# Kernel optimization log

Measured on AMD Instinct MI355X. Metric: run time of the kernel, lower is better.

Reference implementation:

```python
import jax, jax.numpy as jnp
import numpy as np

V = 49152      # HEALPix nside=64 pixel count
B = 2
FIN = 32
FOUT = 64
K = 8          # Chebyshev kernel_size
DEG = 8        # neighbors per pixel (plus self-loop -> 9 nnz/row)
G = 8          # GroupNorm num_groups
EPS = 1e-5
SLOPE = 0.1    # LeakyReLU negative slope


def setup_inputs() -> dict:
    key = jax.random.key(0)
    ks = jax.random.split(key, 4)
    rng = np.random.default_rng(0)
    # sparse Laplacian in COO: 8 random neighbors + self-loop per node
    row = np.repeat(np.arange(V, dtype=np.int32), DEG + 1)
    nbrs = rng.integers(0, V, size=(V, DEG))
    col = np.concatenate([nbrs, np.arange(V)[:, None]], axis=1).astype(np.int32).reshape(-1)
    vals = (rng.standard_normal(V * (DEG + 1)).astype(np.float32)) * 0.1
    x = jax.random.normal(ks[0], (B, V, FIN), dtype=jnp.float32)
    W1 = jax.random.normal(ks[1], (K, FIN, FOUT), dtype=jnp.float32) * 0.05
    W2 = jax.random.normal(ks[2], (K, FOUT, FOUT), dtype=jnp.float32) * 0.05
    Wr = jax.random.normal(ks[3], (K, FIN, FOUT), dtype=jnp.float32) * 0.05
    zeros = jnp.zeros((FOUT,), dtype=jnp.float32)
    ones = jnp.ones((FOUT,), dtype=jnp.float32)
    return {
        "x": x,
        "lap_vals": jnp.asarray(vals),
        "lap_row": jnp.asarray(row),
        "lap_col": jnp.asarray(col),
        "W1": W1, "b1": zeros, "g1": ones, "be1": zeros,
        "W2": W2, "b2": zeros, "g2": ones, "be2": zeros,
        "Wr": Wr, "br": zeros,
    }


def _spmm(vals, row, col, z):
    # L @ z for COO Laplacian; z: [V, D]
    return jax.ops.segment_sum(vals[:, None] * z[col], row, num_segments=V)


def _cheb_conv(x, vals, row, col, W, b):
    # x: [B, V, Fin], W: [K, Fin, Fout] -> [B, V, Fout]
    Bb, Vv, F = x.shape
    x0 = jnp.transpose(x, (1, 0, 2)).reshape(Vv, Bb * F)  # [V, B*F]
    xs = [x0, _spmm(vals, row, col, x0)]
    for _ in range(K - 2):
        xs.append(2.0 * _spmm(vals, row, col, xs[-1]) - xs[-2])
    Xk = jnp.stack(xs, 0).reshape(K, Vv, Bb, F)
    Xk = jnp.transpose(Xk, (2, 1, 0, 3))  # [B, V, K, F]
    return jnp.einsum('bvkf,kfo->bvo', Xk, W) + b


def _group_norm(x, gamma, beta):
    # equivalent to nn.GroupNorm applied on x.permute(0,2,1): normalize over (C/G, V)
    Bb, Vv, C = x.shape
    xg = x.reshape(Bb, Vv, G, C // G)
    mu = xg.mean(axis=(1, 3), keepdims=True)
    var = xg.var(axis=(1, 3), keepdims=True)
    xn = ((xg - mu) * jax.lax.rsqrt(var + EPS)).reshape(Bb, Vv, C)
    return xn * gamma + beta


def _block(x, vals, row, col, W, b, gamma, beta):
    h = _cheb_conv(x, vals, row, col, W, b)
    h = _group_norm(h, gamma, beta)
    return jax.nn.leaky_relu(h, SLOPE)  # out_channels > 1 -> LeakyReLU(0.1)


def reference(x, lap_vals, lap_row, lap_col, W1, b1, g1, be1, W2, b2, g2, be2, Wr, br):
    h = _block(x, lap_vals, lap_row, lap_col, W1, b1, g1, be1)
    h = _block(h, lap_vals, lap_row, lap_col, W2, b2, g2, be2)
    res = _cheb_conv(x, lap_vals, lap_row, lap_col, Wr, br)  # in != out -> res_conv
    return h + res
```

## Files before the change

kernel.cpp:

```cpp
#include <hip/hip_runtime.h>
#include <hip/hip_bf16.h>

#define V 49152
#define NNZ 9
#define EPSV 1e-5f
#define SLOPE 0.1f

typedef __attribute__((ext_vector_type(8))) short bf16x8;
typedef __attribute__((ext_vector_type(4))) float f32x4;

__device__ __forceinline__ float lo2f(unsigned u) { return __uint_as_float(u << 16); }
__device__ __forceinline__ float hi2f(unsigned u) { return __uint_as_float(u & 0xffff0000u); }
__device__ __forceinline__ unsigned short f2us(float f) {
    __hip_bfloat16 h = __float2bfloat16(f);
    return *(unsigned short*)&h;
}
__device__ __forceinline__ float us2f(unsigned short u) { return __uint_as_float(((unsigned)u) << 16); }
__device__ __forceinline__ unsigned pk2(float a, float b) {
    return ((unsigned)f2us(a)) | (((unsigned)f2us(b)) << 16);
}

__device__ __forceinline__ void gload_lds16(const void* g, void* l) {
    __builtin_amdgcn_global_load_lds((__attribute__((address_space(1))) void*)g,
                                     (__attribute__((address_space(3))) void*)l, 16, 0, 0);
}

__global__ __launch_bounds__(256) void prep_k(
    const float* __restrict__ W1, const float* __restrict__ Wr, const float* __restrict__ W2,
    unsigned short* __restrict__ Wt1, unsigned short* __restrict__ Wtr, unsigned short* __restrict__ Wt2,
    float* __restrict__ part)
{
    int i = blockIdx.x * 256 + threadIdx.x;
    if (i < 32768) {
        int kk = i >> 12, rem = i & 4095, o = rem >> 6, f = rem & 63;
        Wt2[i] = f2us(W2[kk * 4096 + f * 64 + o]);
    } else if (i < 49152) {
        int j = i - 32768;
        int kk = j >> 11, rem = j & 2047, o = rem >> 5, f = rem & 31;
        Wt1[j] = f2us(W1[kk * 2048 + f * 64 + o]);
    } else if (i < 65536) {
        int j = i - 49152;
        int kk = j >> 11, rem = j & 2047, o = rem >> 5, f = rem & 31;
        Wtr[j] = f2us(Wr[kk * 2048 + f * 64 + o]);
    } else if (i < 66560) {
        part[i - 65536] = 0.f;
    }
}

__global__ __launch_bounds__(256) void reorder_k(const float* __restrict__ x, unsigned* __restrict__ t0) {
    int idx = blockIdx.x * 256 + threadIdx.x;
    int v = idx >> 5, j2 = idx & 31;
    int b = j2 >> 4, f0 = (j2 & 15) * 2;
    const float* p = x + ((size_t)b * V + v) * 32 + f0;
    t0[idx] = pk2(p[0], p[1]);
}

template<int THR, bool FIRST>
__global__ __launch_bounds__(256) void spmm_step(
    const uint4* __restrict__ zc, const uint4* __restrict__ zp, uint4* __restrict__ zn,
    const float* __restrict__ vals, const int* __restrict__ col)
{
    constexpr int L4 = THR * 2;
    int tid = blockIdx.x * 256 + threadIdx.x;
    int v = tid / THR;
    int c = (tid - v * THR) * 2;
    int base = v * NNZ;
    float t[16];
    #pragma unroll
    for (int i = 0; i < 16; ++i) t[i] = 0.f;
    #pragma unroll
    for (int n = 0; n < NNZ; ++n) {
        float a = vals[base + n];
        int cc = col[base + n];
        const uint4* p = zc + (size_t)cc * L4 + c;
        uint4 u0 = p[0];
        uint4 u1 = p[1];
        t[0] += a * lo2f(u0.x); t[1] += a * hi2f(u0.x);
        t[2] += a * lo2f(u0.y); t[3] += a * hi2f(u0.y);
        t[4] += a * lo2f(u0.z); t[5] += a * hi2f(u0.z);
        t[6] += a * lo2f(u0.w); t[7] += a * hi2f(u0.w);
        t[8]  += a * lo2f(u1.x); t[9]  += a * hi2f(u1.x);
        t[10] += a * lo2f(u1.y); t[11] += a * hi2f(u1.y);
        t[12] += a * lo2f(u1.z); t[13] += a * hi2f(u1.z);
        t[14] += a * lo2f(u1.w); t[15] += a * hi2f(u1.w);
    }
    if (!FIRST) {
        const uint4* pp = zp + (size_t)v * L4 + c;
        uint4 p0 = pp[0];
        uint4 p1 = pp[1];
        t[0] = 2.f*t[0] - lo2f(p0.x); t[1] = 2.f*t[1] - hi2f(p0.x);
        t[2] = 2.f*t[2] - lo2f(p0.y); t[3] = 2.f*t[3] - hi2f(p0.y);
        t[4] = 2.f*t[4] - lo2f(p0.z); t[5] = 2.f*t[5] - hi2f(p0.z);
        t[6] = 2.f*t[6] - lo2f(p0.w); t[7] = 2.f*t[7] - hi2f(p0.w);
        t[8]  = 2.f*t[8]  - lo2f(p1.x); t[9]  = 2.f*t[9]  - hi2f(p1.x);
        t[10] = 2.f*t[10] - lo2f(p1.y); t[11] = 2.f*t[11] - hi2f(p1.y);
        t[12] = 2.f*t[12] - lo2f(p1.z); t[13] = 2.f*t[13] - hi2f(p1.z);
        t[14] = 2.f*t[14] - lo2f(p1.w); t[15] = 2.f*t[15] - hi2f(p1.w);
    }
    uint4 r0, r1;
    r0.x = pk2(t[0], t[1]);  r0.y = pk2(t[2], t[3]);
    r0.z = pk2(t[4], t[5]);  r0.w = pk2(t[6], t[7]);
    r1.x = pk2(t[8], t[9]);  r1.y = pk2(t[10], t[11]);
    r1.z = pk2(t[12], t[13]); r1.w = pk2(t[14], t[15]);
    uint4* q = zn + (size_t)v * L4 + c;
    q[0] = r0;
    q[1] = r1;
}

template<int F, int NKK, bool DUAL, bool INIT, bool FINAL>
__global__ __launch_bounds__(256) void mfma_gemm(
    const unsigned short* __restrict__ T,
    const unsigned short* __restrict__ WtA, const unsigned short* __restrict__ WtB,
    const float* __restrict__ biasA, const float* __restrict__ biasB,
    unsigned short* __restrict__ ACC, float* __restrict__ resOut,
    float* __restrict__ part)
{
    constexpr int CPR = F / 4;
    constexpr int FH = F / 32;
    __shared__ unsigned short tile[NKK * 64 * 2 * F];

    int wv = threadIdx.x >> 6, lane = threadIdx.x & 63;
    int quad = lane >> 4, l15 = lane & 15;
    int v0 = blockIdx.x * 64;
    int ot = wv;

    #pragma unroll
    for (int i = 0; i < 16; ++i) {
        int s = (i * 4 + wv) * 64 + lane;
        int kk = s / (64 * CPR);
        int ws = s - kk * 64 * CPR;
        int row = ws / CPR;
        int cl = ws - row * CPR;
        int cg = (cl & ~7) | ((cl & 7) ^ (row & 7));
        const unsigned short* gp = T + ((size_t)kk * V + v0 + row) * (2 * F) + cg * 8;
        gload_lds16(gp, tile + (size_t)(i * 4 + wv) * 64 * 8);
    }

    bf16x8 bw[NKK][FH];
    bf16x8 bd[NKK][FH];
    #pragma unroll
    for (int kk = 0; kk < NKK; ++kk) {
        #pragma unroll
        for (int fh = 0; fh < FH; ++fh) {
            size_t brow = ((size_t)kk * 64 + ot * 16 + l15) * F + fh * 32 + quad * 8;
            bw[kk][fh] = *(const bf16x8*)(const void*)(WtA + brow);
            if constexpr (DUAL) bd[kk][fh] = *(const bf16x8*)(const void*)(WtB + brow);
        }
    }

    f32x4 acc[4][2];
    f32x4 accd[4][2];
    #pragma unroll
    for (int m = 0; m < 4; ++m)
        #pragma unroll
        for (int b = 0; b < 2; ++b) {
            acc[m][b] = (f32x4){0.f, 0.f, 0.f, 0.f};
            if constexpr (DUAL) accd[m][b] = (f32x4){0.f, 0.f, 0.f, 0.f};
        }

    __syncthreads();

    #pragma unroll
    for (int kk = 0; kk < NKK; ++kk) {
        #pragma unroll
        for (int fh = 0; fh < FH; ++fh) {
            #pragma unroll
            for (int m = 0; m < 4; ++m) {
                int r = m * 16 + l15;
                int rx = r & 7;
                const unsigned short* rbase = tile + ((size_t)kk * 64 + r) * 2 * F;
                #pragma unroll
                for (int b = 0; b < 2; ++b) {
                    int c0 = b * (CPR / 2) + fh * 4 + quad;
                    int s0 = (c0 & ~7) | ((c0 & 7) ^ rx);
                    bf16x8 a = *(const bf16x8*)(const void*)(rbase + s0 * 8);
                    acc[m][b] = __builtin_amdgcn_mfma_f32_16x16x32_bf16(a, bw[kk][fh], acc[m][b], 0, 0, 0);
                    if constexpr (DUAL)
                        accd[m][b] = __builtin_amdgcn_mfma_f32_16x16x32_bf16(a, bd[kk][fh], accd[m][b], 0, 0, 0);
                }
            }
        }
    }

    float* sS = (float*)tile;
    float* sQ = sS + 128;
    if constexpr (FINAL) {
        __syncthreads();
    }

    int o = ot * 16 + l15;
    #pragma unroll
    for (int b = 0; b < 2; ++b) {
        float bia = FINAL ? biasA[o] : 0.f;
        float s = 0.f, q = 0.f;
        #pragma unroll
        for (int m = 0; m < 4; ++m) {
            #pragma unroll
            for (int rr = 0; rr < 4; ++rr) {
                int v = v0 + m * 16 + quad * 4 + rr;
                size_t idx = ((size_t)b * V + v) * 64 + o;
                float val = acc[m][b][rr] + bia;
                if constexpr (!INIT) val += us2f(ACC[idx]);
                ACC[idx] = f2us(val);
                if constexpr (FINAL) { s += val; q += val * val; }
                if constexpr (DUAL) resOut[idx] = accd[m][b][rr] + biasB[o];
            }
        }
        if constexpr (FINAL) {
            s += __shfl_xor(s, 16); s += __shfl_xor(s, 32);
            q += __shfl_xor(q, 16); q += __shfl_xor(q, 32);
            if (quad == 0) { sS[b * 64 + o] = s; sQ[b * 64 + o] = q; }
        }
    }
    if constexpr (FINAL) {
        __syncthreads();
        if (threadIdx.x < 128) {
            int b = threadIdx.x >> 6, oo = threadIdx.x & 63;
            atomicAdd(&part[(b * 64 + oo) * 2], sS[b * 64 + oo]);
            atomicAdd(&part[(b * 64 + oo) * 2 + 1], sQ[b * 64 + oo]);
        }
    }
}

__global__ __launch_bounds__(64) void gn_finalize(const float* __restrict__ part, float* __restrict__ stats) {
    int t = threadIdx.x;
    if (t < 16) {
        int b = t >> 3, g = t & 7;
        float s = 0.f, q = 0.f;
        for (int c = g * 8; c < g * 8 + 8; ++c) {
            s += part[(b * 64 + c) * 2];
            q += part[(b * 64 + c) * 2 + 1];
        }
        const float N = (float)V * 8.f;
        float mean = s / N;
        float var = q / N - mean * mean;
        stats[t * 2] = mean;
        stats[t * 2 + 1] = rsqrtf(var + EPSV);
    }
}

__global__ __launch_bounds__(256) void gn_apply(const unsigned short* __restrict__ ACC,
                                                const float* __restrict__ stats,
                                                const float* __restrict__ gamma, const float* __restrict__ beta,
                                                unsigned* __restrict__ zout) {
    int idx = blockIdx.x * 256 + threadIdx.x;
    int v = idx >> 6, j2 = idx & 63;
    int b = j2 >> 5, o0 = (j2 & 31) * 2;
    float y[2];
    #pragma unroll
    for (int i = 0; i < 2; ++i) {
        int o = o0 + i;
        int bg = b * 8 + (o >> 3);
        float mean = stats[bg * 2], rstd = stats[bg * 2 + 1];
        float val = us2f(ACC[((size_t)b * V + v) * 64 + o]);
        float t = (val - mean) * rstd * gamma[o] + beta[o];
        y[i] = t > 0.f ? t : SLOPE * t;
    }
    zout[idx] = pk2(y[0], y[1]);
}

__global__ __launch_bounds__(256) void final_out(const unsigned short* __restrict__ ACC,
                                                 float* outres,
                                                 const float* __restrict__ stats,
                                                 const float* __restrict__ gamma, const float* __restrict__ beta) {
    int idx = blockIdx.x * 256 + threadIdx.x;
    int o = idx & 63;
    int b = idx >= V * 64 ? 1 : 0;
    int bg = b * 8 + (o >> 3);
    float mean = stats[bg * 2], rstd = stats[bg * 2 + 1];
    float y = (us2f(ACC[idx]) - mean) * rstd * gamma[o] + beta[o];
    y = y > 0.f ? y : SLOPE * y;
    outres[idx] = y + outres[idx];
}

extern "C" void kernel_launch(void* const* d_in, const int* in_sizes, int n_in,
                              void* d_out, int out_size, void* d_ws, size_t ws_size,
                              hipStream_t stream) {
    const float* x    = (const float*)d_in[0];
    const float* vals = (const float*)d_in[1];
    const int*   col  = (const int*)d_in[3];
    const float* W1   = (const float*)d_in[4];
    const float* b1   = (const float*)d_in[5];
    const float* g1   = (const float*)d_in[6];
    const float* be1  = (const float*)d_in[7];
    const float* W2   = (const float*)d_in[8];
    const float* b2   = (const float*)d_in[9];
    const float* g2   = (const float*)d_in[10];
    const float* be2  = (const float*)d_in[11];
    const float* Wr   = (const float*)d_in[12];
    const float* br   = (const float*)d_in[13];
    float* out = (float*)d_out;

    unsigned short* TS  = (unsigned short*)d_ws;
    unsigned short* ACC = TS + (size_t)4 * V * 128;
    unsigned short* Wt1 = ACC + (size_t)2 * V * 64;
    unsigned short* Wtr = Wt1 + 8 * 64 * 32;
    unsigned short* Wt2 = Wtr + 8 * 64 * 32;
    float* PART1 = (float*)(Wt2 + 8 * 64 * 64);
    float* PART2 = PART1 + 256;
    float* ST1   = PART2 + 256;
    float* ST2   = ST1 + 32;

    prep_k<<<260, 256, 0, stream>>>(W1, Wr, W2, Wt1, Wtr, Wt2, PART1);

    uint4* T1s[8];
    for (int k = 0; k < 8; ++k) T1s[k] = (uint4*)(TS + (size_t)k * V * 64);

    reorder_k<<<V * 32 / 256, 256, 0, stream>>>(x, (unsigned*)T1s[0]);
    spmm_step<4, true><<<V * 4 / 256, 256, 0, stream>>>(T1s[0], nullptr, T1s[1], vals, col);
    for (int k = 2; k < 8; ++k)
        spmm_step<4, false><<<V * 4 / 256, 256, 0, stream>>>(T1s[k-1], T1s[k-2], T1s[k], vals, col);

    mfma_gemm<32, 8, true, true, true><<<V / 64, 256, 0, stream>>>(
        TS, Wt1, Wtr, b1, br, ACC, out, PART1);
    gn_finalize<<<1, 64, 0, stream>>>(PART1, ST1);

    uint4* T2s[4];
    for (int k = 0; k < 4; ++k) T2s[k] = (uint4*)(TS + (size_t)k * V * 128);

    gn_apply<<<V * 64 / 256, 256, 0, stream>>>(ACC, ST1, g1, be1, (unsigned*)T2s[0]);
    spmm_step<8, true><<<V * 8 / 256, 256, 0, stream>>>(T2s[0], nullptr, T2s[1], vals, col);
    spmm_step<8, false><<<V * 8 / 256, 256, 0, stream>>>(T2s[1], T2s[0], T2s[2], vals, col);
    spmm_step<8, false><<<V * 8 / 256, 256, 0, stream>>>(T2s[2], T2s[1], T2s[3], vals, col);

    mfma_gemm<64, 4, false, true, false><<<V / 64, 256, 0, stream>>>(
        TS, Wt2, nullptr, b2, nullptr, ACC, nullptr, PART2);

    spmm_step<8, false><<<V * 8 / 256, 256, 0, stream>>>(T2s[3], T2s[2], T2s[0], vals, col);
    spmm_step<8, false><<<V * 8 / 256, 256, 0, stream>>>(T2s[0], T2s[3], T2s[1], vals, col);
    spmm_step<8, false><<<V * 8 / 256, 256, 0, stream>>>(T2s[1], T2s[0], T2s[2], vals, col);
    spmm_step<8, false><<<V * 8 / 256, 256, 0, stream>>>(T2s[2], T2s[1], T2s[3], vals, col);

    mfma_gemm<64, 4, false, false, true><<<V / 64, 256, 0, stream>>>(
        TS, Wt2 + 4 * 64 * 64, nullptr, b2, nullptr, ACC, nullptr, PART2);
    gn_finalize<<<1, 64, 0, stream>>>(PART2, ST2);

    final_out<<<2 * V * 64 / 256, 256, 0, stream>>>(ACC, out, ST2, g2, be2);
}
```

Baseline: 413.7 us.

## Stage GEMM epilogue through LDS for coalesced stores and group-level stat atomics

The MFMA GEMM epilogue now writes accumulator fragments into a padded LDS buffer, then re-reads them row-wise so each thread loads, updates and stores eight contiguous bf16 values (and float4 for the residual output), replacing scattered 2-byte and 4-byte global accesses. GroupNorm partial sums are reduced per group in shared memory and flushed with 16 atomics per stat instead of 128 per-channel atomics, which shrinks the partial buffer and simplifies gn_finalize. It adds an extra barrier and LDS round trip, and prep_k's zeroing of PART1 must still cover the repacked buffer layout.

Measured after the change: 387.1 us. 1.07x faster.

```diff
diff --git a/kernel.cpp b/kernel.cpp
--- a/kernel.cpp
+++ b/kernel.cpp
@@ -117,7 +117,16 @@
 {
     constexpr int CPR = F / 4;
     constexpr int FH = F / 32;
-    __shared__ unsigned short tile[NKK * 64 * 2 * F];
+    constexpr int RST = 68;
+    constexpr int STAGE_SH = NKK * 64 * 2 * F;
+    constexpr int TRANS_SH = (DUAL ? 2 : 1) * 2 * 64 * RST * 2;
+    constexpr int SH = STAGE_SH > TRANS_SH ? STAGE_SH : TRANS_SH;
+    __shared__ unsigned short shraw[SH];
+    __shared__ float sGrp[32];
+
+    unsigned short* tile = shraw;
+    float* accbuf  = (float*)shraw;
+    float* dualbuf = accbuf + 2 * 64 * RST;
 
     int wv = threadIdx.x >> 6, lane = threadIdx.x & 63;
     int quad = lane >> 4, l15 = lane & 15;
@@ -182,42 +191,71 @@
         }
     }
 
-    float* sS = (float*)tile;
-    float* sQ = sS + 128;
+    __syncthreads();
+
+    int o = ot * 16 + l15;
+    float bia = FINAL ? biasA[o] : 0.f;
+    float biaB = DUAL ? biasB[o] : 0.f;
+    #pragma unroll
+    for (int m = 0; m < 4; ++m) {
+        #pragma unroll
+        for (int b = 0; b < 2; ++b) {
+            #pragma unroll
+            for (int rr = 0; rr < 4; ++rr) {
+                int r = m * 16 + quad * 4 + rr;
+                accbuf[(b * 64 + r) * RST + o] = acc[m][b][rr] + bia;
+                if constexpr (DUAL) dualbuf[(b * 64 + r) * RST + o] = accd[m][b][rr] + biaB;
+            }
+        }
+    }
+    if constexpr (FINAL) {
+        if (threadIdx.x < 32) sGrp[threadIdx.x] = 0.f;
+    }
+    __syncthreads();
+
+    #pragma unroll
+    for (int j = 0; j < 4; ++j) {
+        int cid = threadIdx.x + 256 * j;
+        int g = cid & 7, r = (cid >> 3) & 63, b = cid >> 9;
+        int o0 = g * 8;
+        const float* src = accbuf + (b * 64 + r) * RST + o0;
+        float e[8];
+        #pragma unroll
+        for (int i = 0; i < 8; ++i) e[i] = src[i];
+        size_t gidx = ((size_t)b * V + v0 + r) * 64 + o0;
+        if constexpr (!INIT) {
+            uint4 old = *(const uint4*)(const void*)(ACC + gidx);
+            e[0] += lo2f(old.x); e[1] += hi2f(old.x);
+            e[2] += lo2f(old.y); e[3] += hi2f(old.y);
+            e[4] += lo2f(old.z); e[5] += hi2f(old.z);
+            e[6] += lo2f(old.w); e[7] += hi2f(old.w);
+        }
+        uint4 pk;
+        pk.x = pk2(e[0], e[1]); pk.y = pk2(e[2], e[3]);
+        pk.z = pk2(e[4], e[5]); pk.w = pk2(e[6], e[7]);
+        *(uint4*)(void*)(ACC + gidx) = pk;
+        if constexpr (FINAL) {
+            float s = 0.f, q = 0.f;
+            #pragma unroll
+            for (int i = 0; i < 8; ++i) { s += e[i]; q += e[i] * e[i]; }
+            atomicAdd(&sGrp[b * 8 + g], s);
+            atomicAdd(&sGrp[16 + b * 8 + g], q);
+        }
+    }
+    if constexpr (DUAL) {
+        #pragma unroll
+        for (int j = 0; j < 8; ++j) {
+            int cid = threadIdx.x + 256 * j;
+            int oc = cid & 15, r = (cid >> 4) & 63, b = cid >> 10;
+            float4 vv = *(const float4*)(const void*)(dualbuf + (b * 64 + r) * RST + oc * 4);
+            *(float4*)(void*)(resOut + ((size_t)b * V + v0 + r) * 64 + oc * 4) = vv;
+        }
+    }
     if constexpr (FINAL) {
         __syncthreads();
-    }
-
-    int o = ot * 16 + l15;
-    #pragma unroll
-    for (int b = 0; b < 2; ++b) {
-        float bia = FINAL ? biasA[o] : 0.f;
-        float s = 0.f, q = 0.f;
-        #pragma unroll
-        for (int m = 0; m < 4; ++m) {
-            #pragma unroll
-            for (int rr = 0; rr < 4; ++rr) {
-                int v = v0 + m * 16 + quad * 4 + rr;
-                size_t idx = ((size_t)b * V + v) * 64 + o;
-                float val = acc[m][b][rr] + bia;
-                if constexpr (!INIT) val += us2f(ACC[idx]);
-                ACC[idx] = f2us(val);
-                if constexpr (FINAL) { s += val; q += val * val; }
-                if constexpr (DUAL) resOut[idx] = accd[m][b][rr] + biasB[o];
-            }
-        }
-        if constexpr (FINAL) {
-            s += __shfl_xor(s, 16); s += __shfl_xor(s, 32);
-            q += __shfl_xor(q, 16); q += __shfl_xor(q, 32);
-            if (quad == 0) { sS[b * 64 + o] = s; sQ[b * 64 + o] = q; }
-        }
-    }
-    if constexpr (FINAL) {
-        __syncthreads();
-        if (threadIdx.x < 128) {
-            int b = threadIdx.x >> 6, oo = threadIdx.x & 63;
-            atomicAdd(&part[(b * 64 + oo) * 2], sS[b * 64 + oo]);
-            atomicAdd(&part[(b * 64 + oo) * 2 + 1], sQ[b * 64 + oo]);
+        if (threadIdx.x < 16) {
+            atomicAdd(&part[threadIdx.x * 2],     sGrp[threadIdx.x]);
+            atomicAdd(&part[threadIdx.x * 2 + 1], sGrp[16 + threadIdx.x]);
         }
     }
 }
@@ -225,15 +263,9 @@
 __global__ __launch_bounds__(64) void gn_finalize(const float* __restrict__ part, float* __restrict__ stats) {
     int t = threadIdx.x;
     if (t < 16) {
-        int b = t >> 3, g = t & 7;
-        float s = 0.f, q = 0.f;
-        for (int c = g * 8; c < g * 8 + 8; ++c) {
-            s += part[(b * 64 + c) * 2];
-            q += part[(b * 64 + c) * 2 + 1];
-        }
         const float N = (float)V * 8.f;
-        float mean = s / N;
-        float var = q / N - mean * mean;
+        float mean = part[t * 2] / N;
+        float var = part[t * 2 + 1] / N - mean * mean;
         stats[t * 2] = mean;
         stats[t * 2 + 1] = rsqrtf(var + EPSV);
     }
@@ -297,8 +329,8 @@
     unsigned short* Wtr = Wt1 + 8 * 64 * 32;
     unsigned short* Wt2 = Wtr + 8 * 64 * 32;
     float* PART1 = (float*)(Wt2 + 8 * 64 * 64);
-    float* PART2 = PART1 + 256;
-    float* ST1   = PART2 + 256;
+    float* PART2 = PART1 + 32;
+    float* ST1   = PART2 + 32;
     float* ST2   = ST1 + 32;
 
     prep_k<<<260, 256, 0, stream>>>(W1, Wr, W2, Wt1, Wtr, Wt2, PART1);
```
